# Performance work log

Measured on AMD Instinct MI355X. Metric: run time of the kernel, lower is better.

Reference implementation:

```python
import jax, jax.numpy as jnp
import numpy as np

IN_F, OUT_F = 4096, 4096
IGS, OGS = 8, 1          # in_group_size, out_group_size
NCB, CBS = 1, 65536      # num_codebooks, codebook_size (2**16)
NIG, NOG = IN_F // IGS, OUT_F // OGS


def setup_inputs() -> dict:
    key = jax.random.key(0)
    k1, k2, k3, k4, k5 = jax.random.split(key, 5)
    x = jax.random.normal(k1, (4, 2048, IN_F), jnp.float32)
    codes = jax.random.randint(k2, (NOG, NIG, NCB), 0, CBS, dtype=jnp.int32)
    codebooks = jax.random.normal(k3, (NCB, CBS, OGS, IGS), jnp.float32) * 0.05
    scales = jax.random.uniform(k4, (NOG, 1, 1, 1), jnp.float32, 0.5, 1.5)
    bias = jax.random.normal(k5, (OUT_F,), jnp.float32) * 0.01
    return {"x": x, "codes": codes, "codebooks": codebooks, "scales": scales, "bias": bias}


def _dequantize_weight(codes, codebooks, scales):
    # codes: [nog, nig, ncb] int; codebooks: [ncb, cbs, ogs, igs]
    ncb, cbs, ogs, igs = codebooks.shape
    nog, nig, _ = codes.shape
    flat = codebooks.reshape(ncb, cbs, ogs * igs)
    # embedding_bag(mode='sum'): gather each codebook's vector and sum over codebooks
    gathered = flat[jnp.arange(ncb)[None, None, :], codes]  # [nog, nig, ncb, ogs*igs]
    w = gathered.sum(axis=2).reshape(nog, nig, ogs, igs)
    w = w * scales  # scales broadcasts over [nog, nig, ogs, igs]
    # [nog, nig, ogs, igs] -> [nog, ogs, nig, igs] -> [out_features, in_features]
    return w.swapaxes(1, 2).reshape(nog * ogs, nig * igs)


def reference(x, codes, codebooks, scales, bias):
    W = _dequantize_weight(codes, codebooks, scales)  # [OUT_F, IN_F]
    return x @ W.T + bias
```

## Files before the change

kernel.cpp:

```cpp
#include <hip/hip_runtime.h>
#include <hip/hip_bf16.h>

#define M_DIM 8192
#define N_DIM 4096
#define K_DIM 4096
#define NOG 4096
#define NIG 512

typedef __bf16 bf16x8 __attribute__((ext_vector_type(8)));
typedef float f32x4 __attribute__((ext_vector_type(4)));
typedef short short8 __attribute__((ext_vector_type(8)));

typedef const __attribute__((address_space(1))) void* as1_cvoid_p;
typedef __attribute__((address_space(3))) void* as3_void_p;

__device__ __forceinline__ unsigned short f2bf(float f) {
  union { float f; unsigned u; } c; c.f = f;
  unsigned u = c.u;
  return (unsigned short)((u + 0x7fffu + ((u >> 16) & 1u)) >> 16);
}

__global__ __launch_bounds__(256) void cvt_x_kernel(const float* __restrict__ x,
                                                    unsigned short* __restrict__ xb,
                                                    int n8) {
  int i = blockIdx.x * blockDim.x + threadIdx.x;
  int stride = gridDim.x * blockDim.x;
  for (; i < n8; i += stride) {
    const float4* p = (const float4*)(x) + (size_t)i * 2;
    float4 a = p[0], b = p[1];
    short8 o;
    o[0] = (short)f2bf(a.x); o[1] = (short)f2bf(a.y);
    o[2] = (short)f2bf(a.z); o[3] = (short)f2bf(a.w);
    o[4] = (short)f2bf(b.x); o[5] = (short)f2bf(b.y);
    o[6] = (short)f2bf(b.z); o[7] = (short)f2bf(b.w);
    ((short8*)xb)[i] = o;
  }
}

__global__ __launch_bounds__(256) void dequant_kernel(const int* __restrict__ codes,
                                                      const float* __restrict__ cb,
                                                      unsigned short* __restrict__ wb) {
  int idx = blockIdx.x * blockDim.x + threadIdx.x;
  int code = codes[idx];
  const float4* p = (const float4*)(cb + (size_t)code * 8);
  float4 a = p[0], b = p[1];
  short8 o;
  o[0] = (short)f2bf(a.x); o[1] = (short)f2bf(a.y);
  o[2] = (short)f2bf(a.z); o[3] = (short)f2bf(a.w);
  o[4] = (short)f2bf(b.x); o[5] = (short)f2bf(b.y);
  o[6] = (short)f2bf(b.z); o[7] = (short)f2bf(b.w);
  ((short8*)wb)[idx] = o;
}


#define BAR() __builtin_amdgcn_s_barrier()
#define SB() __builtin_amdgcn_sched_barrier(0)
#define PRIO1() __builtin_amdgcn_s_setprio(1)
#define PRIO0() __builtin_amdgcn_s_setprio(0)
#define LGKM(N_) asm volatile("s_waitcnt lgkmcnt(" #N_ ")" ::: "memory")
#define VMC(N_) asm volatile("s_waitcnt vmcnt(" #N_ ")" ::: "memory")

#define STAGE_A(slot_, h_, kt_) do { \
  _Pragma("unroll") for (int i_ = 0; i_ < 2; ++i_) { \
    const unsigned short* src_ = Ag + (size_t)(sa_roff[i_] + (h_) * 64) * 4096 + (unsigned)((kt_) + sa_koff[i_]); \
    __builtin_amdgcn_global_load_lds((as1_cvoid_p)src_, \
      (as3_void_p)(smem + (slot_) * 32768 + sa_lds[i_] + (h_) * 4096), 16, 0, 0); \
  } } while (0)

#define STAGE_B(slot_, h_, kt_) do { \
  _Pragma("unroll") for (int i_ = 0; i_ < 2; ++i_) { \
    const unsigned short* src_ = Bg + (size_t)(sb_roff[i_] + (h_) * 32) * 4096 + (unsigned)((kt_) + sb_koff[i_]); \
    __builtin_amdgcn_global_load_lds((as1_cvoid_p)src_, \
      (as3_void_p)(smem + 65536 + (slot_) * 32768 + sb_lds[i_] + (h_) * 2048), 16, 0, 0); \
  } } while (0)

#define LDA_Q(q_, ma_, slot_) \
  _Pragma("unroll") for (int j_ = 0; j_ < 2; ++j_) \
  _Pragma("unroll") for (int kk_ = 0; kk_ < 2; ++kk_) \
    af[(q_) * 2 + j_][kk_] = *(const bf16x8*)(smem + (slot_) * 32768 + aRd + ((ma_) * 4 + (q_) * 2 + j_) * 1024 + kk_ * 16384);

#define LDB(n0_, dst_, slot_) \
  _Pragma("unroll") for (int n_ = 0; n_ < 2; ++n_) \
  _Pragma("unroll") for (int kk_ = 0; kk_ < 2; ++kk_) \
    dst_[n_][kk_] = *(const bf16x8*)(smem + (slot_) * 32768 + bRd + ((n0_) + n_) * 1024 + kk_ * 16384);

#define MM_Q(base_, q_, nb_, bfr_) \
  _Pragma("unroll") for (int j_ = 0; j_ < 2; ++j_) \
  _Pragma("unroll") for (int n_ = 0; n_ < 2; ++n_) \
  _Pragma("unroll") for (int kk_ = 0; kk_ < 2; ++kk_) \
    acc[(base_) + (q_) * 2 + j_][(nb_) + n_] = __builtin_amdgcn_mfma_f32_16x16x32_bf16( \
        af[(q_) * 2 + j_][kk_], bfr_[n_][kk_], acc[(base_) + (q_) * 2 + j_][(nb_) + n_], 0, 0, 0);

#define GROUP(SLOT_, MODE_, KT_) do { \
   \
  LDA_Q(0, 0, SLOT_); LDA_Q(1, 0, SLOT_); LDB(2, bf1, SLOT_); \
  if ((MODE_) >= 1) STAGE_A((SLOT_) ^ 1, 1, (KT_) + 64); \
  LGKM(8); SB(); PRIO1(); MM_Q(0, 0, 0, bf0); \
  LGKM(4); SB(); MM_Q(0, 1, 0, bf0); PRIO0(); \
  if ((MODE_) >= 1) { VMC(8); } else { VMC(0); } \
  BAR(); \
   \
  if ((MODE_) == 2) STAGE_A(SLOT_, 0, (KT_) + 128); \
  PRIO1(); MM_Q(0, 0, 2, bf1); MM_Q(0, 1, 2, bf1); PRIO0(); \
  if ((MODE_) == 2) { VMC(8); } else if ((MODE_) == 1) { VMC(6); } \
  BAR(); \
   \
  LDA_Q(0, 1, SLOT_); LDA_Q(1, 1, SLOT_); \
  if ((MODE_) == 2) STAGE_B(SLOT_, 0, (KT_) + 128); \
  LGKM(4); SB(); PRIO1(); MM_Q(4, 0, 0, bf0); \
  LGKM(0); SB(); MM_Q(4, 1, 0, bf0); PRIO0(); \
  if ((MODE_) == 2) { VMC(6); } else if ((MODE_) == 1) { VMC(2); } \
  BAR(); \
   \
  if ((MODE_) >= 1) { LDB(0, bf0, (SLOT_) ^ 1); } \
  if ((MODE_) == 2) STAGE_B(SLOT_, 1, (KT_) + 128); \
  PRIO1(); MM_Q(4, 0, 2, bf1); MM_Q(4, 1, 2, bf1); PRIO0(); \
} while (0)

__global__ __launch_bounds__(512) void gemm8_kernel(
    const unsigned short* __restrict__ A,
    const unsigned short* __restrict__ B,
    const float* __restrict__ scales,
    const float* __restrict__ bias,
    float* __restrict__ C) {
  extern __shared__ char smem[];

  const int bid = blockIdx.x;
  const int swz = (bid & 7) * 64 + (bid >> 3);
  const int bm = swz >> 4;
  const int bn = swz & 15;

  const int tid = threadIdx.x;
  const int w = tid >> 6;
  const int l = tid & 63;
  const int wr = w >> 2;
  const int wcol = w & 3;

  const int llog = l ^ (((l >> 5) & 1) << 1);
  int sa_roff[2], sa_koff[2], sa_lds[2];
  int sb_roff[2], sb_koff[2], sb_lds[2];
#pragma unroll
  for (int i = 0; i < 2; ++i) {
    int u = w * 2 + i;
    int panel = u >> 3;
    int rbA = (u >> 2) & 1, chA = u & 3;
    sa_roff[i] = rbA * 128 + chA * 16 + (llog >> 2);
    sa_koff[i] = panel * 32 + (llog & 3) * 8;
    sa_lds[i] = panel * 16384 + rbA * 8192 + chA * 1024;
    int bb = (u >> 1) & 3, hk = u & 1;
    sb_roff[i] = bb * 64 + hk * 16 + (llog >> 2);
    sb_koff[i] = panel * 32 + (llog & 3) * 8;
    sb_lds[i] = panel * 16384 + bb * 4096 + hk * 1024;
  }

  const unsigned short* Ag = A + (size_t)bm * 256 * 4096;
  const unsigned short* Bg = B + (size_t)bn * 256 * 4096;

  const int xr = ((l >> 4) * 16) ^ (((l >> 3) & 1) << 5);
  const int aRd = (wr * 128 + (l & 15)) * 64 + xr;
  const int bRd = 65536 + (wcol * 64 + (l & 15)) * 64 + xr;

  f32x4 acc[8][4];
#pragma unroll
  for (int m = 0; m < 8; ++m)
#pragma unroll
    for (int n = 0; n < 4; ++n) acc[m][n] = (f32x4){0.f, 0.f, 0.f, 0.f};

  bf16x8 af[4][2], bf0[2][2], bf1[2][2];

  STAGE_A(0, 0, 0); STAGE_B(0, 0, 0); STAGE_B(0, 1, 0);
  STAGE_A(0, 1, 0);
  STAGE_A(1, 0, 64); STAGE_B(1, 0, 64); STAGE_B(1, 1, 64);
  VMC(8);
  BAR();
  LDB(0, bf0, 0);

  int kt = 0;
  for (int j = 0; j < 31; ++j) {
    GROUP(0, 2, kt);
    GROUP(1, 2, kt + 64);
    kt += 128;
  }
  GROUP(0, 1, kt);
  GROUP(1, 0, kt + 64);

  const int row0 = bm * 256 + wr * 128 + ((l >> 4) << 2);
  const int col0 = bn * 256 + wcol * 64 + (l & 15);
#pragma unroll
  for (int n = 0; n < 4; ++n) {
    const int col = col0 + n * 16;
    const float s = scales[col];
    const float bv = bias[col];
#pragma unroll
    for (int m = 0; m < 8; ++m) {
      f32x4 v = acc[m][n];
      const int r = row0 + m * 16;
#pragma unroll
      for (int j = 0; j < 4; ++j)
        C[(size_t)(r + j) * 4096 + col] = v[j] * s + bv;
    }
  }
}

extern "C" void kernel_launch(void* const* d_in, const int* in_sizes, int n_in,
                              void* d_out, int out_size, void* d_ws, size_t ws_size,
                              hipStream_t stream) {
  const float* x = (const float*)d_in[0];
  const int* codes = (const int*)d_in[1];
  const float* cb = (const float*)d_in[2];
  const float* scales = (const float*)d_in[3];
  const float* bias = (const float*)d_in[4];
  float* out = (float*)d_out;

  unsigned short* xb = (unsigned short*)d_ws;
  unsigned short* wb = (unsigned short*)((char*)d_ws + (size_t)M_DIM * K_DIM * 2);

  hipFuncSetAttribute((const void*)gemm8_kernel,
                      hipFuncAttributeMaxDynamicSharedMemorySize, 131072);

  cvt_x_kernel<<<4096, 256, 0, stream>>>(x, xb, (M_DIM * K_DIM) / 8);
  dequant_kernel<<<(NOG * NIG) / 256, 256, 0, stream>>>(codes, cb, wb);
  gemm8_kernel<<<dim3((M_DIM / 256) * (N_DIM / 256)), 512, 131072, stream>>>(
      xb, wb, scales, bias, out);
}
```

Measured before the change: 262.9 us.

## Software-pipeline LDS fragment loads across MFMA quarters in GEMM group

Reorders the per-group schedule so LDS reads for A and B fragments are issued one quarter ahead and interleaved between MFMA batches, including prefetching the next slot's A fragments at the end of the group. The goal is to hide LDS latency behind matrix-core work instead of stalling on lgkmcnt before each MFMA block. It adds more sched barriers and changes the wait counts, which risks register pressure or incorrect wait counts if the accounting is off.

```diff
diff --git a/kernel.cpp b/kernel.cpp
--- a/kernel.cpp
+++ b/kernel.cpp
@@ -93,28 +93,36 @@
 
 #define GROUP(SLOT_, MODE_, KT_) do { \
    \
-  LDA_Q(0, 0, SLOT_); LDA_Q(1, 0, SLOT_); LDB(2, bf1, SLOT_); \
+  LDB(2, bf1, SLOT_); SB(); \
+  LGKM(4); SB(); \
+  PRIO1(); MM_Q(0, 0, 0, bf0); MM_Q(0, 1, 0, bf0); PRIO0(); SB(); \
   if ((MODE_) >= 1) STAGE_A((SLOT_) ^ 1, 1, (KT_) + 64); \
-  LGKM(8); SB(); PRIO1(); MM_Q(0, 0, 0, bf0); \
-  LGKM(4); SB(); MM_Q(0, 1, 0, bf0); PRIO0(); \
   if ((MODE_) >= 1) { VMC(8); } else { VMC(0); } \
   BAR(); \
    \
+  LGKM(0); SB(); \
+  PRIO1(); MM_Q(0, 0, 2, bf1); PRIO0(); SB(); \
+  LDA_Q(0, 1, SLOT_); SB(); \
+  PRIO1(); MM_Q(0, 1, 2, bf1); PRIO0(); SB(); \
+  LDA_Q(1, 1, SLOT_); SB(); \
   if ((MODE_) == 2) STAGE_A(SLOT_, 0, (KT_) + 128); \
-  PRIO1(); MM_Q(0, 0, 2, bf1); MM_Q(0, 1, 2, bf1); PRIO0(); \
-  if ((MODE_) == 2) { VMC(8); } else if ((MODE_) == 1) { VMC(6); } \
   BAR(); \
    \
-  LDA_Q(0, 1, SLOT_); LDA_Q(1, 1, SLOT_); \
+  LGKM(4); SB(); \
+  PRIO1(); MM_Q(4, 0, 0, bf0); PRIO0(); SB(); \
+  LGKM(0); SB(); \
+  PRIO1(); MM_Q(4, 1, 0, bf0); PRIO0(); SB(); \
   if ((MODE_) == 2) STAGE_B(SLOT_, 0, (KT_) + 128); \
-  LGKM(4); SB(); PRIO1(); MM_Q(4, 0, 0, bf0); \
-  LGKM(0); SB(); MM_Q(4, 1, 0, bf0); PRIO0(); \
   if ((MODE_) == 2) { VMC(6); } else if ((MODE_) == 1) { VMC(2); } \
   BAR(); \
    \
-  if ((MODE_) >= 1) { LDB(0, bf0, (SLOT_) ^ 1); } \
+  PRIO1(); MM_Q(4, 0, 2, bf1); PRIO0(); SB(); \
+  if ((MODE_) >= 1) { LDA_Q(0, 0, (SLOT_) ^ 1); LDB(0, bf0, (SLOT_) ^ 1); } \
+  SB(); \
+  PRIO1(); MM_Q(4, 1, 2, bf1); PRIO0(); SB(); \
+  if ((MODE_) >= 1) { LDA_Q(1, 0, (SLOT_) ^ 1); } \
+  SB(); \
   if ((MODE_) == 2) STAGE_B(SLOT_, 1, (KT_) + 128); \
-  PRIO1(); MM_Q(4, 0, 2, bf1); MM_Q(4, 1, 2, bf1); PRIO0(); \
 } while (0)
 
 __global__ __launch_bounds__(512) void gemm8_kernel(
@@ -173,7 +181,7 @@
   STAGE_A(1, 0, 64); STAGE_B(1, 0, 64); STAGE_B(1, 1, 64);
   VMC(8);
   BAR();
-  LDB(0, bf0, 0);
+  LDA_Q(0, 0, 0); SB(); LDB(0, bf0, 0); SB(); LDA_Q(1, 0, 0); SB();
 
   int kt = 0;
   for (int j = 0; j < 31; ++j) {
```

New measurement: 263.1 us. No clear change (+0.1%).

## Load B fragments directly from global to registers and triple-buffer A in LDS

Applied to the files above, without the earlier changes.

The B operand is no longer staged through LDS. Each wave now loads its B fragments straight from global memory into registers, and A moves to a 3-slot LDS ring with a reworked group schedule and less shared memory. The intent is to cut LDS traffic and barriers for B and to deepen A prefetch. The risk is that B reads from global are less coalesced and duplicated across the two row-waves, and direct global latency may stall the MFMAs.

```diff
diff --git a/kernel.cpp b/kernel.cpp
--- a/kernel.cpp
+++ b/kernel.cpp
@@ -67,22 +67,15 @@
       (as3_void_p)(smem + (slot_) * 32768 + sa_lds[i_] + (h_) * 4096), 16, 0, 0); \
   } } while (0)
 
-#define STAGE_B(slot_, h_, kt_) do { \
-  _Pragma("unroll") for (int i_ = 0; i_ < 2; ++i_) { \
-    const unsigned short* src_ = Bg + (size_t)(sb_roff[i_] + (h_) * 32) * 4096 + (unsigned)((kt_) + sb_koff[i_]); \
-    __builtin_amdgcn_global_load_lds((as1_cvoid_p)src_, \
-      (as3_void_p)(smem + 65536 + (slot_) * 32768 + sb_lds[i_] + (h_) * 2048), 16, 0, 0); \
-  } } while (0)
+#define LOAD_B(dst_, half_, kt_) \
+  _Pragma("unroll") for (int n_ = 0; n_ < 2; ++n_) \
+  _Pragma("unroll") for (int kk_ = 0; kk_ < 2; ++kk_) \
+    dst_[n_][kk_] = *(const bf16x8*)(Bl + (size_t)((half_) * 2 + n_) * 16 * 4096 + (unsigned)((kt_) + kk_ * 32));
 
 #define LDA_Q(q_, ma_, slot_) \
   _Pragma("unroll") for (int j_ = 0; j_ < 2; ++j_) \
   _Pragma("unroll") for (int kk_ = 0; kk_ < 2; ++kk_) \
     af[(q_) * 2 + j_][kk_] = *(const bf16x8*)(smem + (slot_) * 32768 + aRd + ((ma_) * 4 + (q_) * 2 + j_) * 1024 + kk_ * 16384);
-
-#define LDB(n0_, dst_, slot_) \
-  _Pragma("unroll") for (int n_ = 0; n_ < 2; ++n_) \
-  _Pragma("unroll") for (int kk_ = 0; kk_ < 2; ++kk_) \
-    dst_[n_][kk_] = *(const bf16x8*)(smem + (slot_) * 32768 + bRd + ((n0_) + n_) * 1024 + kk_ * 16384);
 
 #define MM_Q(base_, q_, nb_, bfr_) \
   _Pragma("unroll") for (int j_ = 0; j_ < 2; ++j_) \
@@ -91,30 +84,28 @@
     acc[(base_) + (q_) * 2 + j_][(nb_) + n_] = __builtin_amdgcn_mfma_f32_16x16x32_bf16( \
         af[(q_) * 2 + j_][kk_], bfr_[n_][kk_], acc[(base_) + (q_) * 2 + j_][(nb_) + n_], 0, 0, 0);
 
-#define GROUP(SLOT_, MODE_, KT_) do { \
-   \
-  LDA_Q(0, 0, SLOT_); LDA_Q(1, 0, SLOT_); LDB(2, bf1, SLOT_); \
-  if ((MODE_) >= 1) STAGE_A((SLOT_) ^ 1, 1, (KT_) + 64); \
-  LGKM(8); SB(); PRIO1(); MM_Q(0, 0, 0, bf0); \
-  LGKM(4); SB(); MM_Q(0, 1, 0, bf0); PRIO0(); \
-  if ((MODE_) >= 1) { VMC(8); } else { VMC(0); } \
+#define GROUP(SC_, SN_, SS_, MODE_, KT_) do { \
   BAR(); \
    \
-  if ((MODE_) == 2) STAGE_A(SLOT_, 0, (KT_) + 128); \
-  PRIO1(); MM_Q(0, 0, 2, bf1); MM_Q(0, 1, 2, bf1); PRIO0(); \
-  if ((MODE_) == 2) { VMC(8); } else if ((MODE_) == 1) { VMC(6); } \
+  LOAD_B(bf1, 1, KT_); SB(); \
+  if ((MODE_) == 2) { STAGE_A(SS_, 0, (KT_) + 128); STAGE_A(SS_, 1, (KT_) + 128); } \
+  SB(); \
+  if ((MODE_) == 2) { VMC(8); } else { VMC(4); } \
   BAR(); \
-   \
-  LDA_Q(0, 1, SLOT_); LDA_Q(1, 1, SLOT_); \
-  if ((MODE_) == 2) STAGE_B(SLOT_, 0, (KT_) + 128); \
+  LGKM(4); SB(); PRIO1(); MM_Q(0, 0, 0, bf0); \
+  LGKM(0); SB(); MM_Q(0, 1, 0, bf0); PRIO0(); SB(); \
+   \
+  if ((MODE_) == 2) { VMC(4); } else { VMC(0); } \
+  SB(); PRIO1(); MM_Q(0, 0, 2, bf1); MM_Q(0, 1, 2, bf1); PRIO0(); SB(); \
+  LDA_Q(0, 1, SC_); SB(); LDA_Q(1, 1, SC_); SB(); \
+   \
   LGKM(4); SB(); PRIO1(); MM_Q(4, 0, 0, bf0); \
-  LGKM(0); SB(); MM_Q(4, 1, 0, bf0); PRIO0(); \
-  if ((MODE_) == 2) { VMC(6); } else if ((MODE_) == 1) { VMC(2); } \
-  BAR(); \
-   \
-  if ((MODE_) >= 1) { LDB(0, bf0, (SLOT_) ^ 1); } \
-  if ((MODE_) == 2) STAGE_B(SLOT_, 1, (KT_) + 128); \
-  PRIO1(); MM_Q(4, 0, 2, bf1); MM_Q(4, 1, 2, bf1); PRIO0(); \
+  LGKM(0); SB(); MM_Q(4, 1, 0, bf0); PRIO0(); SB(); \
+   \
+  if ((MODE_) >= 1) { LOAD_B(bf0, 0, (KT_) + 64); } \
+  SB(); PRIO1(); MM_Q(4, 0, 2, bf1); MM_Q(4, 1, 2, bf1); PRIO0(); SB(); \
+  if ((MODE_) >= 1) { LDA_Q(0, 0, SN_); SB(); LDA_Q(1, 0, SN_); } \
+  SB(); \
 } while (0)
 
 __global__ __launch_bounds__(512) void gemm8_kernel(
@@ -138,7 +129,6 @@
 
   const int llog = l ^ (((l >> 5) & 1) << 1);
   int sa_roff[2], sa_koff[2], sa_lds[2];
-  int sb_roff[2], sb_koff[2], sb_lds[2];
 #pragma unroll
   for (int i = 0; i < 2; ++i) {
     int u = w * 2 + i;
@@ -147,18 +137,13 @@
     sa_roff[i] = rbA * 128 + chA * 16 + (llog >> 2);
     sa_koff[i] = panel * 32 + (llog & 3) * 8;
     sa_lds[i] = panel * 16384 + rbA * 8192 + chA * 1024;
-    int bb = (u >> 1) & 3, hk = u & 1;
-    sb_roff[i] = bb * 64 + hk * 16 + (llog >> 2);
-    sb_koff[i] = panel * 32 + (llog & 3) * 8;
-    sb_lds[i] = panel * 16384 + bb * 4096 + hk * 1024;
   }
 
   const unsigned short* Ag = A + (size_t)bm * 256 * 4096;
-  const unsigned short* Bg = B + (size_t)bn * 256 * 4096;
+  const unsigned short* Bl = B + ((size_t)bn * 256 + wcol * 64 + (l & 15)) * 4096 + ((l >> 4) * 8);
 
   const int xr = ((l >> 4) * 16) ^ (((l >> 3) & 1) << 5);
   const int aRd = (wr * 128 + (l & 15)) * 64 + xr;
-  const int bRd = 65536 + (wcol * 64 + (l & 15)) * 64 + xr;
 
   f32x4 acc[8][4];
 #pragma unroll
@@ -168,21 +153,25 @@
 
   bf16x8 af[4][2], bf0[2][2], bf1[2][2];
 
-  STAGE_A(0, 0, 0); STAGE_B(0, 0, 0); STAGE_B(0, 1, 0);
-  STAGE_A(0, 1, 0);
-  STAGE_A(1, 0, 64); STAGE_B(1, 0, 64); STAGE_B(1, 1, 64);
+  STAGE_A(0, 0, 0); STAGE_A(0, 1, 0);
+  STAGE_A(1, 0, 64); STAGE_A(1, 1, 64);
+  LOAD_B(bf0, 0, 0); SB();
   VMC(8);
   BAR();
-  LDB(0, bf0, 0);
+  LDA_Q(0, 0, 0); SB(); LDA_Q(1, 0, 0); SB();
 
   int kt = 0;
-  for (int j = 0; j < 31; ++j) {
-    GROUP(0, 2, kt);
-    GROUP(1, 2, kt + 64);
-    kt += 128;
-  }
-  GROUP(0, 1, kt);
-  GROUP(1, 0, kt + 64);
+  for (int j = 0; j < 20; ++j) {
+    GROUP(0, 1, 2, 2, kt);
+    GROUP(1, 2, 0, 2, kt + 64);
+    GROUP(2, 0, 1, 2, kt + 128);
+    kt += 192;
+  }
+  GROUP(0, 1, 2, 2, 3840);
+  GROUP(1, 2, 0, 2, 3904);
+  GROUP(2, 0, 1, 1, 3968);
+  GROUP(0, 1, 2, 0, 4032);
+  SB();
 
   const int row0 = bm * 256 + wr * 128 + ((l >> 4) << 2);
   const int col0 = bn * 256 + wcol * 64 + (l & 15);
@@ -216,10 +205,10 @@
   unsigned short* wb = (unsigned short*)((char*)d_ws + (size_t)M_DIM * K_DIM * 2);
 
   hipFuncSetAttribute((const void*)gemm8_kernel,
-                      hipFuncAttributeMaxDynamicSharedMemorySize, 131072);
+                      hipFuncAttributeMaxDynamicSharedMemorySize, 98304);
 
   cvt_x_kernel<<<4096, 256, 0, stream>>>(x, xb, (M_DIM * K_DIM) / 8);
   dequant_kernel<<<(NOG * NIG) / 256, 256, 0, stream>>>(codes, cb, wb);
-  gemm8_kernel<<<dim3((M_DIM / 256) * (N_DIM / 256)), 512, 131072, stream>>>(
+  gemm8_kernel<<<dim3((M_DIM / 256) * (N_DIM / 256)), 512, 98304, stream>>>(
       xb, wb, scales, bias, out);
 }
```

Result: slower. 373.0 us (+41.9%).
